# Kernel optimization log

Hardware: AMD Instinct MI355X
Metric: run time of the kernel (lower is better)

Reference implementation:

```python
import jax, jax.numpy as jnp
import numpy as np

COST_CLASS, COST_BBOX, COST_GIOU = 1.0, 5.0, 2.0
NUM_FRAMES, Q_PER_FRAME, NUM_TGT, NUM_CLASSES = 36, 100, 20, 92
B = 64


def box_cxcywh_to_xyxy(b):
    cx, cy, w, h = b[..., 0], b[..., 1], b[..., 2], b[..., 3]
    return jnp.stack([cx - 0.5 * w, cy - 0.5 * h, cx + 0.5 * w, cy + 0.5 * h], axis=-1)


def pairwise_giou(b1, b2):
    # b1: [..., Q, 4], b2: [..., T, 4], xyxy -> giou [..., Q, T]
    area1 = (b1[..., 2] - b1[..., 0]) * (b1[..., 3] - b1[..., 1])
    area2 = (b2[..., 2] - b2[..., 0]) * (b2[..., 3] - b2[..., 1])
    lt = jnp.maximum(b1[..., :, None, :2], b2[..., None, :, :2])
    rb = jnp.minimum(b1[..., :, None, 2:], b2[..., None, :, 2:])
    wh = jnp.clip(rb - lt, 0.0)
    inter = wh[..., 0] * wh[..., 1]
    union = area1[..., :, None] + area2[..., None, :] - inter
    iou = inter / union
    lt_e = jnp.minimum(b1[..., :, None, :2], b2[..., None, :, :2])
    rb_e = jnp.maximum(b1[..., :, None, 2:], b2[..., None, :, 2:])
    wh_e = jnp.clip(rb_e - lt_e, 0.0)
    area_e = wh_e[..., 0] * wh_e[..., 1]
    return iou - (area_e - union) / area_e


def compute_cost(pred_logits, pred_boxes, tgt_labels, tgt_boxes):
    b = pred_logits.shape[0]
    prob = jax.nn.softmax(pred_logits.reshape(b, NUM_FRAMES, Q_PER_FRAME, -1), axis=-1)  # [B,F,Q,C]
    pb = pred_boxes.reshape(b, NUM_FRAMES, Q_PER_FRAME, 4)
    lab = jnp.transpose(tgt_labels, (1, 0, 2))            # [B,F,T]
    tb = jnp.transpose(tgt_boxes, (1, 0, 2, 3))           # [B,F,T,4]
    onehot = jax.nn.one_hot(lab, prob.shape[-1], dtype=prob.dtype)  # [B,F,T,C]
    cost_class = -jnp.einsum('bfqc,bftc->bfqt', prob, onehot)
    cost_bbox = jnp.abs(pb[:, :, :, None, :] - tb[:, :, None, :, :]).sum(-1)  # L1 cdist
    giou = pairwise_giou(box_cxcywh_to_xyxy(pb), box_cxcywh_to_xyxy(tb))
    return COST_CLASS * cost_class + COST_BBOX * cost_bbox - COST_GIOU * giou


def auction_assign(cost):
    # cost [Q, T]; returns obj_of [T]: query index assigned to each target.
    # eps-optimal auction algorithm (replaces scipy linear_sum_assignment).
    Q, T = cost.shape
    benefit = -cost.T  # [T, Q]
    spread = jnp.max(benefit) - jnp.min(benefit) + 1e-6
    eps = spread / 1000.0
    neg_inf = jnp.asarray(-1e30, cost.dtype)

    def cond(s):
        _, _, obj_of, it = s
        return jnp.logical_and(jnp.any(obj_of < 0), it < 20000)

    def body(s):
        price, owner, obj_of, it = s
        unassigned = obj_of < 0                       # [T]
        vals = benefit - price[None, :]               # [T, Q]
        top2v, top2i = jax.lax.top_k(vals, 2)
        best_obj = top2i[:, 0]                        # [T]
        bid = price[best_obj] + (top2v[:, 0] - top2v[:, 1]) + eps
        bid = jnp.where(unassigned, bid, neg_inf)
        best_bid = jnp.full((Q,), neg_inf, cost.dtype).at[best_obj].max(bid)
        pids = jnp.arange(T, dtype=jnp.int32)
        win = unassigned & (bid >= best_bid[best_obj])
        winner = jnp.full((Q,), T, jnp.int32).at[best_obj].min(jnp.where(win, pids, T))
        has_bid = winner < T
        # evict previous owners of objects that received a bid
        evict = jnp.where(has_bid & (owner >= 0), owner, T)
        obj_of = obj_of.at[evict].set(-1, mode='drop')
        qids = jnp.arange(Q, dtype=jnp.int32)
        obj_of = obj_of.at[jnp.where(has_bid, winner, T)].set(jnp.where(has_bid, qids, -1), mode='drop')
        price = jnp.where(has_bid, best_bid, price)
        owner = jnp.where(has_bid, winner, owner)
        return price, owner, obj_of, it + 1

    init = (jnp.zeros((Q,), cost.dtype), jnp.full((Q,), -1, jnp.int32),
            jnp.full((T,), -1, jnp.int32), jnp.int32(0))
    _, _, obj_of, _ = jax.lax.while_loop(cond, body, init)
    return obj_of


def setup_inputs() -> dict:
    key = jax.random.key(0)
    k1, k2, k3, k4 = jax.random.split(key, 4)
    pred_logits = jax.random.normal(k1, (B, NUM_FRAMES * Q_PER_FRAME, NUM_CLASSES), jnp.float32)
    pred_boxes = jax.random.uniform(k2, (B, NUM_FRAMES * Q_PER_FRAME, 4), jnp.float32)
    tgt_labels = jax.random.randint(k3, (NUM_FRAMES, B, NUM_TGT), 0, NUM_CLASSES, jnp.int32)
    tgt_boxes = jax.random.uniform(k4, (NUM_FRAMES, B, NUM_TGT, 4), jnp.float32)
    return {'pred_logits': pred_logits, 'pred_boxes': pred_boxes,
            'tgt_labels': tgt_labels, 'tgt_boxes': tgt_boxes}


def reference(pred_logits, pred_boxes, tgt_labels, tgt_boxes):
    cost = compute_cost(pred_logits, pred_boxes, tgt_labels, tgt_boxes)  # [B,F,Q,T]
    b, f, q, t = cost.shape
    obj_of = jax.vmap(auction_assign)(cost.reshape(b * f, q, t))  # [BF, T]
    order = jnp.argsort(obj_of, axis=-1)  # scipy returns rows ascending
    pred_idx = jnp.take_along_axis(obj_of, order, axis=-1).reshape(b, f, t)
    tgt_idx = order.astype(jnp.int32).reshape(b, f, t)
    return cost, pred_idx, tgt_idx
```

## Files before the change

kernel.cpp:

```cpp
#include <hip/hip_runtime.h>

#define NF 36
#define QN 100
#define TN 20
#define CN 92
#define NB 64
#define BSTR 104

__global__ __launch_bounds__(64) void matcher_kernel(
    const float* __restrict__ logits,
    const float* __restrict__ pboxes,
    const int*   __restrict__ tlabels,
    const float* __restrict__ tboxes,
    float* __restrict__ out_cost,
    float* __restrict__ out_pred,
    float* __restrict__ out_tgt)
{
    const int bf = blockIdx.x;
    const int b  = bf / NF;
    const int f  = bf % NF;
    const int lane = threadIdx.x;

    __shared__ float ben[TN][BSTR];
    __shared__ float price[BSTR];
    __shared__ int   owner[QN];
    __shared__ float bidv[TN];
    __shared__ int   bo[TN];
    __shared__ int   evict[TN];
    __shared__ int   objl[TN];
    __shared__ int   slab[TN];
    __shared__ float tbr[TN][4];
    __shared__ float tbx[TN][4];
    __shared__ float tarea[TN];

    if (lane < TN) {
        const int base = (f * NB + b) * TN + lane;
        slab[lane] = tlabels[base];
        const float* tb = tboxes + (size_t)base * 4;
        float cx = tb[0], cy = tb[1], w = tb[2], h = tb[3];
        tbr[lane][0] = cx; tbr[lane][1] = cy; tbr[lane][2] = w; tbr[lane][3] = h;
        float x1 = cx - 0.5f * w, y1 = cy - 0.5f * h;
        float x2 = cx + 0.5f * w, y2 = cy + 0.5f * h;
        tbx[lane][0] = x1; tbx[lane][1] = y1; tbx[lane][2] = x2; tbx[lane][3] = y2;
        tarea[lane] = (x2 - x1) * (y2 - y1);
        evict[lane] = 0;
    }
    __syncthreads();

    float mn = INFINITY, mx = -INFINITY;
    for (int p = 0; p < 2; ++p) {
        const int q = lane + 64 * p;
        if (q < QN) {
            const size_t row = (size_t)b * (NF * QN) + (size_t)f * QN + q;
            const float* L = logits + row * CN;
            const float4* L4 = reinterpret_cast<const float4*>(L);
            float4 r[23];
            #pragma unroll
            for (int i = 0; i < 23; ++i) r[i] = L4[i];
            float m = -INFINITY;
            #pragma unroll
            for (int i = 0; i < 23; ++i) {
                float4 v = r[i];
                m = fmaxf(m, v.x); m = fmaxf(m, v.y); m = fmaxf(m, v.z); m = fmaxf(m, v.w);
            }
            float s = 0.f;
            #pragma unroll
            for (int i = 0; i < 23; ++i) {
                float4 v = r[i];
                s += expf(v.x - m); s += expf(v.y - m); s += expf(v.z - m); s += expf(v.w - m);
            }

            float4 pbv = reinterpret_cast<const float4*>(pboxes)[row];
            float cx = pbv.x, cy = pbv.y, w = pbv.z, h = pbv.w;
            float px1 = cx - 0.5f * w, py1 = cy - 0.5f * h;
            float px2 = cx + 0.5f * w, py2 = cy + 0.5f * h;
            float a1 = (px2 - px1) * (py2 - py1);

            for (int t = 0; t < TN; ++t) {
                float pc = expf(L[slab[t]] - m) / s;
                float cb = fabsf(cx - tbr[t][0]) + fabsf(cy - tbr[t][1]);
                cb = cb + fabsf(w - tbr[t][2]);
                cb = cb + fabsf(h - tbr[t][3]);
                float ltx = fmaxf(px1, tbx[t][0]), lty = fmaxf(py1, tbx[t][1]);
                float rbx = fminf(px2, tbx[t][2]), rby = fminf(py2, tbx[t][3]);
                float wx = fmaxf(rbx - ltx, 0.f), wy = fmaxf(rby - lty, 0.f);
                float inter = wx * wy;
                float uni = a1 + tarea[t] - inter;
                float iou = inter / uni;
                float ex1 = fminf(px1, tbx[t][0]), ey1 = fminf(py1, tbx[t][1]);
                float ex2 = fmaxf(px2, tbx[t][2]), ey2 = fmaxf(py2, tbx[t][3]);
                float ew = fmaxf(ex2 - ex1, 0.f), eh = fmaxf(ey2 - ey1, 0.f);
                float ae = ew * eh;
                float giou = iou - (ae - uni) / ae;
                float cost = (-pc) + 5.0f * cb - 2.0f * giou;
                ben[t][q] = -cost;
                mn = fminf(mn, cost);
                mx = fmaxf(mx, cost);
            }
        }
    }

    for (int i = lane; i < BSTR; i += 64) price[i] = 0.f;
    for (int i = lane; i < QN; i += 64) owner[i] = -1;
    if (lane < TN) {
        ben[lane][100] = -INFINITY; ben[lane][101] = -INFINITY;
        ben[lane][102] = -INFINITY; ben[lane][103] = -INFINITY;
    }
    __syncthreads();

    #pragma unroll
    for (int off = 32; off > 0; off >>= 1) {
        mn = fminf(mn, __shfl_xor(mn, off, 64));
        mx = fmaxf(mx, __shfl_xor(mx, off, 64));
    }
    const float eps = (((-mn) - (-mx)) + 1e-6f) / 1000.0f;

    {
        float4* dst = reinterpret_cast<float4*>(out_cost + (size_t)bf * (QN * TN));
        for (int i = lane; i < (QN * TN) / 4; i += 64) {
            int k = i * 4;
            int q = k / TN, t0 = k - q * TN;
            float4 v;
            v.x = -ben[t0 + 0][q]; v.y = -ben[t0 + 1][q];
            v.z = -ben[t0 + 2][q]; v.w = -ben[t0 + 3][q];
            dst[i] = v;
        }
    }

    const int myt = lane / 3;
    const int jj  = lane - myt * 3;
    const int q0  = jj * 34;
    const bool is_leader = (lane < 60) && (jj == 0);
    float breg[34];
    {
        const int tt = (lane < 60) ? myt : 0;
        #pragma unroll
        for (int k = 0; k < 34; ++k) breg[k] = ben[tt][q0 + k];
    }
    int myobj = -1;

    for (int it = 0; it < 20000; ++it) {
        unsigned long long U = __ballot(is_leader && (myobj < 0));
        if (U == 0ull) break;

        float v0 = -INFINITY, v1 = -INFINITY; int i0 = q0;
        #pragma unroll
        for (int k = 0; k < 34; ++k) {
            float v = breg[k] - price[q0 + k];
            bool c = v > v0;
            v1 = c ? v0 : fmaxf(v1, v);
            i0 = c ? (q0 + k) : i0;
            v0 = c ? v : v0;
        }
        {
            float av0 = __shfl_down(v0, 1), av1 = __shfl_down(v1, 1);
            int   ai0 = __shfl_down(i0, 1);
            float bv0 = __shfl_down(v0, 2), bv1 = __shfl_down(v1, 2);
            int   bi0 = __shfl_down(i0, 2);
            if (av0 > v0) { v1 = fmaxf(v0, av1); v0 = av0; i0 = ai0; }
            else          { v1 = fmaxf(av0, v1); }
            if (bv0 > v0) { v1 = fmaxf(v0, bv1); v0 = bv0; i0 = bi0; }
            else          { v1 = fmaxf(bv0, v1); }
        }
        float mybid = price[i0] + (v0 - v1) + eps;
        if (is_leader) { bidv[myt] = mybid; bo[myt] = i0; }
        __syncthreads();

        const bool act = is_leader && (((U >> lane) & 1ull) != 0ull);
        if (act) {
            bool lose = false;
            unsigned long long u = U;
            while (u) {
                int pos = __builtin_ctzll(u); u &= (u - 1);
                int t2 = pos / 3;
                if (t2 != myt) {
                    float bv = bidv[t2]; int ob = bo[t2];
                    lose = lose || (ob == i0 && (bv > mybid || (bv == mybid && t2 < myt)));
                }
            }
            if (!lose) {
                int q = i0;
                int old = owner[q];
                owner[q] = myt;
                price[q] = mybid;
                myobj = q;
                if (old >= 0) evict[old] = 1;
            }
        }
        __syncthreads();
        if (is_leader && evict[myt]) { myobj = -1; evict[myt] = 0; }
    }
    __syncthreads();
    if (is_leader) objl[myt] = myobj;
    __syncthreads();

    if (lane < TN) {
        int v = objl[lane];
        int r = 0;
        for (int u = 0; u < TN; ++u) {
            int w = objl[u];
            r += (w < v) || (w == v && u < lane);
        }
        out_pred[(size_t)bf * TN + r] = (float)v;
        out_tgt[(size_t)bf * TN + r]  = (float)lane;
    }
}

extern "C" void kernel_launch(void* const* d_in, const int* in_sizes, int n_in,
                              void* d_out, int out_size, void* d_ws, size_t ws_size,
                              hipStream_t stream) {
    const float* logits  = (const float*)d_in[0];
    const float* pboxes  = (const float*)d_in[1];
    const int*   tlabels = (const int*)d_in[2];
    const float* tboxes  = (const float*)d_in[3];

    float* out = (float*)d_out;
    float* out_cost = out;
    float* out_pred = out + (size_t)NB * NF * QN * TN;
    float* out_tgt  = out_pred + (size_t)NB * NF * TN;

    hipLaunchKernelGGL(matcher_kernel, dim3(NB * NF), dim3(64), 0, stream,
                       logits, pboxes, tlabels, tboxes, out_cost, out_pred, out_tgt);
}
```

Baseline: 180.3 us.

## Restructure auction loop with fast paths for few bidders and atomic conflict resolution

Adds a wave-wide top-2 search for the case of one or two unassigned targets, where all 64 lanes scan one target's row with float4 loads and xor shuffles. With a single bidder the conflict check is skipped entirely. With several bidders the serial scan over the ballot mask is replaced by shared-memory atomicMax/atomicMin on the float bits to pick the winner per object. Rows are padded to 112 and vectorised, with a med3-based top-2 update. This shortens the long tail of auction iterations where few targets remain, at the cost of extra barriers per iteration in the contested path.

```diff
diff --git a/kernel.cpp b/kernel.cpp
--- a/kernel.cpp
+++ b/kernel.cpp
@@ -5,7 +5,12 @@
 #define TN 20
 #define CN 92
 #define NB 64
-#define BSTR 104
+#define BSTR 112
+
+#define TOP2_STEP(VV, IDX) do { \
+    float v_ = (VV); bool c_ = v_ > v0; \
+    float nv1_ = __builtin_amdgcn_fmed3f(v_, v0, v1); \
+    i0 = c_ ? (IDX) : i0; v0 = fmaxf(v0, v_); v1 = nv1_; } while (0)
 
 __global__ __launch_bounds__(64) void matcher_kernel(
     const float* __restrict__ logits,
@@ -21,11 +26,11 @@
     const int f  = bf % NF;
     const int lane = threadIdx.x;
 
-    __shared__ float ben[TN][BSTR];
-    __shared__ float price[BSTR];
+    __shared__ __align__(16) float ben[TN][BSTR];
+    __shared__ __align__(16) float price[BSTR];
     __shared__ int   owner[QN];
-    __shared__ float bidv[TN];
-    __shared__ int   bo[TN];
+    __shared__ int   bbmax[QN];
+    __shared__ int   wmin[QN];
     __shared__ int   evict[TN];
     __shared__ int   objl[TN];
     __shared__ int   slab[TN];
@@ -103,8 +108,9 @@
     for (int i = lane; i < BSTR; i += 64) price[i] = 0.f;
     for (int i = lane; i < QN; i += 64) owner[i] = -1;
     if (lane < TN) {
-        ben[lane][100] = -INFINITY; ben[lane][101] = -INFINITY;
-        ben[lane][102] = -INFINITY; ben[lane][103] = -INFINITY;
+        float4 ninf; ninf.x = ninf.y = ninf.z = ninf.w = -INFINITY;
+        float4* sp = reinterpret_cast<float4*>(&ben[lane][100]);
+        sp[0] = ninf; sp[1] = ninf; sp[2] = ninf;
     }
     __syncthreads();
 
@@ -129,63 +135,102 @@
 
     const int myt = lane / 3;
     const int jj  = lane - myt * 3;
-    const int q0  = jj * 34;
+    const int q0  = jj * 36;
     const bool is_leader = (lane < 60) && (jj == 0);
-    float breg[34];
+    float4 breg4[9];
     {
         const int tt = (lane < 60) ? myt : 0;
+        const float4* bp = reinterpret_cast<const float4*>(&ben[tt][q0]);
         #pragma unroll
-        for (int k = 0; k < 34; ++k) breg[k] = ben[tt][q0 + k];
+        for (int k = 0; k < 9; ++k) breg4[k] = bp[k];
     }
     int myobj = -1;
 
     for (int it = 0; it < 20000; ++it) {
         unsigned long long U = __ballot(is_leader && (myobj < 0));
         if (U == 0ull) break;
-
-        float v0 = -INFINITY, v1 = -INFINITY; int i0 = q0;
-        #pragma unroll
-        for (int k = 0; k < 34; ++k) {
-            float v = breg[k] - price[q0 + k];
-            bool c = v > v0;
-            v1 = c ? v0 : fmaxf(v1, v);
-            i0 = c ? (q0 + k) : i0;
-            v0 = c ? v : v0;
-        }
-        {
-            float av0 = __shfl_down(v0, 1), av1 = __shfl_down(v1, 1);
-            int   ai0 = __shfl_down(i0, 1);
-            float bv0 = __shfl_down(v0, 2), bv1 = __shfl_down(v1, 2);
-            int   bi0 = __shfl_down(i0, 2);
-            if (av0 > v0) { v1 = fmaxf(v0, av1); v0 = av0; i0 = ai0; }
-            else          { v1 = fmaxf(av0, v1); }
-            if (bv0 > v0) { v1 = fmaxf(v0, bv1); v0 = bv0; i0 = bi0; }
-            else          { v1 = fmaxf(bv0, v1); }
-        }
-        float mybid = price[i0] + (v0 - v1) + eps;
-        if (is_leader) { bidv[myt] = mybid; bo[myt] = i0; }
-        __syncthreads();
-
-        const bool act = is_leader && (((U >> lane) & 1ull) != 0ull);
-        if (act) {
-            bool lose = false;
-            unsigned long long u = U;
-            while (u) {
-                int pos = __builtin_ctzll(u); u &= (u - 1);
-                int t2 = pos / 3;
-                if (t2 != myt) {
-                    float bv = bidv[t2]; int ob = bo[t2];
-                    lose = lose || (ob == i0 && (bv > mybid || (bv == mybid && t2 < myt)));
-                }
-            }
-            if (!lose) {
-                int q = i0;
-                int old = owner[q];
-                owner[q] = myt;
-                price[q] = mybid;
-                myobj = q;
-                if (old >= 0) evict[old] = 1;
-            }
+        const int u = __popcll(U);
+
+        int bidq = 0; float bidf = 0.f;
+        if (u > 2) {
+            float v0 = -INFINITY, v1 = -INFINITY; int i0 = q0;
+            const float4* pp = reinterpret_cast<const float4*>(&price[q0]);
+            #pragma unroll
+            for (int k = 0; k < 9; ++k) {
+                float4 bv = breg4[k];
+                float4 pv = pp[k];
+                TOP2_STEP(bv.x - pv.x, q0 + 4*k + 0);
+                TOP2_STEP(bv.y - pv.y, q0 + 4*k + 1);
+                TOP2_STEP(bv.z - pv.z, q0 + 4*k + 2);
+                TOP2_STEP(bv.w - pv.w, q0 + 4*k + 3);
+            }
+            {
+                float av0 = __shfl_down(v0, 1), av1 = __shfl_down(v1, 1);
+                int   ai0 = __shfl_down(i0, 1);
+                float bv0 = __shfl_down(v0, 2), bv1 = __shfl_down(v1, 2);
+                int   bi0 = __shfl_down(i0, 2);
+                if (av0 > v0) { v1 = fmaxf(v0, av1); v0 = av0; i0 = ai0; }
+                else          { v1 = fmaxf(av0, v1); }
+                if (bv0 > v0) { v1 = fmaxf(v0, bv1); v0 = bv0; i0 = bi0; }
+                else          { v1 = fmaxf(bv0, v1); }
+            }
+            bidq = i0;
+            bidf = price[i0] + (v0 - v1) + eps;
+        } else {
+            const int ta = (int)__builtin_ctzll(U) / 3;
+            const int tb = (u == 2) ? (int)__builtin_ctzll(U & (U - 1ull)) / 3 : ta;
+            const int grp = lane >> 5;
+            const int tg  = grp ? tb : ta;
+            const int l   = lane & 31;
+            const int lc  = (l > 25) ? 25 : l;
+            const int qb  = lc * 4;
+            float4 bv = *reinterpret_cast<const float4*>(&ben[tg][qb]);
+            float4 pv = *reinterpret_cast<const float4*>(&price[qb]);
+            float v0 = -INFINITY, v1 = -INFINITY; int i0 = qb;
+            TOP2_STEP(bv.x - pv.x, qb + 0);
+            TOP2_STEP(bv.y - pv.y, qb + 1);
+            TOP2_STEP(bv.z - pv.z, qb + 2);
+            TOP2_STEP(bv.w - pv.w, qb + 3);
+            #pragma unroll
+            for (int s = 16; s >= 1; s >>= 1) {
+                float av0 = __shfl_xor(v0, s), av1 = __shfl_xor(v1, s);
+                int   ai0 = __shfl_xor(i0, s);
+                bool take = (av0 > v0) || (av0 == v0 && ai0 < i0);
+                float nv1 = take ? fmaxf(v0, av1) : fmaxf(v1, av0);
+                v0 = take ? av0 : v0;
+                i0 = take ? ai0 : i0;
+                v1 = nv1;
+            }
+            float bidg = price[i0] + (v0 - v1) + eps;
+            float b0 = __shfl(bidg, 0),  b1 = __shfl(bidg, 32);
+            int   i0a = __shfl(i0, 0),   i0b = __shfl(i0, 32);
+            if (lane == 3 * ta)            { bidq = i0a; bidf = b0; }
+            if (u == 2 && lane == 3 * tb)  { bidq = i0b; bidf = b1; }
+        }
+
+        const bool act = is_leader && (myobj < 0);
+        bool win = false;
+        if (u == 1) {
+            win = act;
+        } else {
+            if (act) { bbmax[bidq] = 0; wmin[bidq] = 64; }
+            __syncthreads();
+            if (act) atomicMax(&bbmax[bidq], __float_as_int(bidf));
+            __syncthreads();
+            bool cand = false;
+            if (act) {
+                cand = (__float_as_int(bidf) >= bbmax[bidq]);
+                if (cand) atomicMin(&wmin[bidq], myt);
+            }
+            __syncthreads();
+            win = cand && (wmin[bidq] == myt);
+        }
+        if (win) {
+            int old = owner[bidq];
+            owner[bidq] = myt;
+            price[bidq] = bidf;
+            myobj = bidq;
+            if (old >= 0) evict[old] = 1;
         }
         __syncthreads();
         if (is_leader && evict[myt]) { myobj = -1; evict[myt] = 0; }
@@ -197,9 +242,9 @@
     if (lane < TN) {
         int v = objl[lane];
         int r = 0;
-        for (int u = 0; u < TN; ++u) {
-            int w = objl[u];
-            r += (w < v) || (w == v && u < lane);
+        for (int u2 = 0; u2 < TN; ++u2) {
+            int w = objl[u2];
+            r += (w < v) || (w == v && u2 < lane);
         }
         out_pred[(size_t)bf * TN + r] = (float)v;
         out_tgt[(size_t)bf * TN + r]  = (float)lane;
```

Measured after the change: 176.7 us. -2.0%, faster.

## Cache top-two auction candidates per target and drop block barriers in bidding

Applied to the files above, without the earlier changes.

The auction loop now caches each unassigned target's best and second-best query, with their benefits and prices. A full 108-entry rescan happens only when the cache is invalidated, either by a price change on the cached second-best query or by the best query losing its margin. Bids are packed into one 64-bit shared word. The owner and evict arrays, plus the __syncthreads calls, are removed, since eviction is now detected by scanning the packed bids of the same single-wavefront block. The layout is widened to 36 queries per lane with float4 loads, and a register-pinning asm is added around the softmax loads. Exchanges: more complex invalidation logic and a reliance on wavefront-synchronous LDS ordering, which could subtly change assignment results if the cache or ordering assumptions are wrong.

```diff
diff --git a/kernel.cpp b/kernel.cpp
--- a/kernel.cpp
+++ b/kernel.cpp
@@ -5,7 +5,31 @@
 #define TN 20
 #define CN 92
 #define NB 64
-#define BSTR 104
+#define BSTR 112
+
+#define SCAN6(BV, PV, IDX) do { \
+    float v_ = (BV) - (PV); \
+    bool c_ = v_ > v0; \
+    bool d_ = v_ > v1; \
+    float nv1_ = __builtin_amdgcn_fmed3f(v_, v0, v1); \
+    i1 = c_ ? i0 : (d_ ? (IDX) : i1); \
+    b1 = c_ ? b0 : (d_ ? (BV) : b1); \
+    v1 = nv1_; \
+    i0 = c_ ? (IDX) : i0; \
+    b0 = c_ ? (BV) : b0; \
+    v0 = fmaxf(v0, v_); } while (0)
+
+#define MERGE6(NV0, NI0, NB0, NV1, NI1, NB1) do { \
+    bool t_  = (NV0) > v0; \
+    bool s1_ = (NV1) > v0; \
+    bool s2_ = (NV0) > v1; \
+    float mv1_ = t_ ? (s1_ ? (NV1) : v0) : (s2_ ? (NV0) : v1); \
+    int   mi1_ = t_ ? (s1_ ? (NI1) : i0) : (s2_ ? (NI0) : i1); \
+    float mb1_ = t_ ? (s1_ ? (NB1) : b0) : (s2_ ? (NB0) : b1); \
+    v0 = t_ ? (NV0) : v0; \
+    i0 = t_ ? (NI0) : i0; \
+    b0 = t_ ? (NB0) : b0; \
+    v1 = mv1_; i1 = mi1_; b1 = mb1_; } while (0)
 
 __global__ __launch_bounds__(64) void matcher_kernel(
     const float* __restrict__ logits,
@@ -21,12 +45,9 @@
     const int f  = bf % NF;
     const int lane = threadIdx.x;
 
-    __shared__ float ben[TN][BSTR];
-    __shared__ float price[BSTR];
-    __shared__ int   owner[QN];
-    __shared__ float bidv[TN];
-    __shared__ int   bo[TN];
-    __shared__ int   evict[TN];
+    __shared__ __align__(16) float ben[TN][BSTR];
+    __shared__ __align__(16) float price[BSTR];
+    __shared__ unsigned long long bid2[TN];
     __shared__ int   objl[TN];
     __shared__ int   slab[TN];
     __shared__ float tbr[TN][4];
@@ -43,7 +64,6 @@
         float x2 = cx + 0.5f * w, y2 = cy + 0.5f * h;
         tbx[lane][0] = x1; tbx[lane][1] = y1; tbx[lane][2] = x2; tbx[lane][3] = y2;
         tarea[lane] = (x2 - x1) * (y2 - y1);
-        evict[lane] = 0;
     }
     __syncthreads();
 
@@ -57,6 +77,10 @@
             float4 r[23];
             #pragma unroll
             for (int i = 0; i < 23; ++i) r[i] = L4[i];
+            #pragma unroll
+            for (int i = 0; i < 23; ++i) {
+                asm volatile("" : "+v"(r[i].x), "+v"(r[i].y), "+v"(r[i].z), "+v"(r[i].w));
+            }
             float m = -INFINITY;
             #pragma unroll
             for (int i = 0; i < 23; ++i) {
@@ -101,10 +125,10 @@
     }
 
     for (int i = lane; i < BSTR; i += 64) price[i] = 0.f;
-    for (int i = lane; i < QN; i += 64) owner[i] = -1;
     if (lane < TN) {
-        ben[lane][100] = -INFINITY; ben[lane][101] = -INFINITY;
-        ben[lane][102] = -INFINITY; ben[lane][103] = -INFINITY;
+        float4 ninf; ninf.x = ninf.y = ninf.z = ninf.w = -INFINITY;
+        float4* sp = reinterpret_cast<float4*>(&ben[lane][100]);
+        sp[0] = ninf; sp[1] = ninf; sp[2] = ninf;
     }
     __syncthreads();
 
@@ -129,66 +153,96 @@
 
     const int myt = lane / 3;
     const int jj  = lane - myt * 3;
-    const int q0  = jj * 34;
+    const int q0  = jj * 36;
     const bool is_leader = (lane < 60) && (jj == 0);
-    float breg[34];
+    float4 breg4[9];
     {
         const int tt = (lane < 60) ? myt : 0;
+        const float4* bp = reinterpret_cast<const float4*>(&ben[tt][q0]);
         #pragma unroll
-        for (int k = 0; k < 34; ++k) breg[k] = ben[tt][q0 + k];
+        for (int k = 0; k < 9; ++k) breg4[k] = bp[k];
     }
     int myobj = -1;
+
+    float cv0 = 0.f, cv1 = 0.f, cb0 = 0.f, cb1 = 0.f, cp0 = 0.f;
+    int ci0 = 0, ci1 = 0;
+    bool cval = false;
 
     for (int it = 0; it < 20000; ++it) {
         unsigned long long U = __ballot(is_leader && (myobj < 0));
         if (U == 0ull) break;
-
-        float v0 = -INFINITY, v1 = -INFINITY; int i0 = q0;
-        #pragma unroll
-        for (int k = 0; k < 34; ++k) {
-            float v = breg[k] - price[q0 + k];
-            bool c = v > v0;
-            v1 = c ? v0 : fmaxf(v1, v);
-            i0 = c ? (q0 + k) : i0;
-            v0 = c ? v : v0;
-        }
-        {
-            float av0 = __shfl_down(v0, 1), av1 = __shfl_down(v1, 1);
-            int   ai0 = __shfl_down(i0, 1);
-            float bv0 = __shfl_down(v0, 2), bv1 = __shfl_down(v1, 2);
-            int   bi0 = __shfl_down(i0, 2);
-            if (av0 > v0) { v1 = fmaxf(v0, av1); v0 = av0; i0 = ai0; }
-            else          { v1 = fmaxf(av0, v1); }
-            if (bv0 > v0) { v1 = fmaxf(v0, bv1); v0 = bv0; i0 = bi0; }
-            else          { v1 = fmaxf(bv0, v1); }
-        }
-        float mybid = price[i0] + (v0 - v1) + eps;
-        if (is_leader) { bidv[myt] = mybid; bo[myt] = i0; }
-        __syncthreads();
-
-        const bool act = is_leader && (((U >> lane) & 1ull) != 0ull);
-        if (act) {
-            bool lose = false;
-            unsigned long long u = U;
-            while (u) {
-                int pos = __builtin_ctzll(u); u &= (u - 1);
+        unsigned long long R = __ballot(is_leader && (myobj < 0) && !cval);
+
+        if (R != 0ull) {
+            const bool doscan = (lane < 60) && (((R >> (3 * myt)) & 1ull) != 0ull);
+            float v0 = -INFINITY, v1 = -INFINITY, b0 = 0.f, b1 = 0.f;
+            int i0 = q0, i1 = q0;
+            if (doscan) {
+                const float4* pp = reinterpret_cast<const float4*>(&price[q0]);
+                #pragma unroll
+                for (int k = 0; k < 9; ++k) {
+                    float4 bv = breg4[k];
+                    float4 pv = pp[k];
+                    SCAN6(bv.x, pv.x, q0 + 4*k + 0);
+                    SCAN6(bv.y, pv.y, q0 + 4*k + 1);
+                    SCAN6(bv.z, pv.z, q0 + 4*k + 2);
+                    SCAN6(bv.w, pv.w, q0 + 4*k + 3);
+                }
+            }
+            {
+                float av0 = __shfl_down(v0, 1), av1 = __shfl_down(v1, 1);
+                float ab0 = __shfl_down(b0, 1), ab1 = __shfl_down(b1, 1);
+                int   ai0 = __shfl_down(i0, 1), ai1 = __shfl_down(i1, 1);
+                float bv0 = __shfl_down(v0, 2), bv1 = __shfl_down(v1, 2);
+                float bb0 = __shfl_down(b0, 2), bb1 = __shfl_down(b1, 2);
+                int   bi0 = __shfl_down(i0, 2), bi1 = __shfl_down(i1, 2);
+                MERGE6(av0, ai0, ab0, av1, ai1, ab1);
+                MERGE6(bv0, bi0, bb0, bv1, bi1, bb1);
+            }
+            if (is_leader && (((R >> lane) & 1ull) != 0ull)) {
+                cv0 = v0; ci0 = i0; cb0 = b0;
+                cv1 = v1; ci1 = i1; cb1 = b1;
+                cp0 = price[ci0];
+                cval = true;
+            }
+        }
+
+        const bool active = is_leader && (myobj < 0);
+        const int   mybidq = ci0;
+        const float mybid  = cp0 + (cv0 - cv1) + eps;
+        if (active) {
+            bid2[myt] = ((unsigned long long)__float_as_uint(mybid) << 32) | (unsigned)mybidq;
+        }
+
+        if (is_leader) {
+            bool lose = false, hit0 = false, kill = false, ev = false;
+            float np0 = -INFINITY;
+            unsigned long long uu = U;
+            while (uu) {
+                int pos = (int)__builtin_ctzll(uu); uu &= uu - 1ull;
                 int t2 = pos / 3;
-                if (t2 != myt) {
-                    float bv = bidv[t2]; int ob = bo[t2];
-                    lose = lose || (ob == i0 && (bv > mybid || (bv == mybid && t2 < myt)));
-                }
-            }
-            if (!lose) {
-                int q = i0;
-                int old = owner[q];
-                owner[q] = myt;
-                price[q] = mybid;
-                myobj = q;
-                if (old >= 0) evict[old] = 1;
-            }
-        }
-        __syncthreads();
-        if (is_leader && evict[myt]) { myobj = -1; evict[myt] = 0; }
+                unsigned long long pk = bid2[t2];
+                int q2 = (int)(unsigned)(pk & 0xffffffffull);
+                float f2 = __uint_as_float((unsigned)(pk >> 32));
+                lose = lose || (active && q2 == mybidq &&
+                                (f2 > mybid || (f2 == mybid && t2 < myt)));
+                ev = ev || (q2 == myobj);
+                bool h0 = (q2 == ci0);
+                np0 = h0 ? fmaxf(np0, f2) : np0;
+                hit0 = hit0 || h0;
+                kill = kill || (q2 == ci1);
+            }
+            if (active && !lose) {
+                myobj = mybidq;
+                price[mybidq] = mybid;
+            } else if (ev) {
+                myobj = -1;
+            }
+            if (cval) {
+                if (hit0) { cp0 = np0; cv0 = cb0 - cp0; }
+                if (kill || (hit0 && !(cv0 > cv1))) cval = false;
+            }
+        }
     }
     __syncthreads();
     if (is_leader) objl[myt] = myobj;
@@ -197,9 +251,9 @@
     if (lane < TN) {
         int v = objl[lane];
         int r = 0;
-        for (int u = 0; u < TN; ++u) {
-            int w = objl[u];
-            r += (w < v) || (w == v && u < lane);
+        for (int u2 = 0; u2 < TN; ++u2) {
+            int w = objl[u2];
+            r += (w < v) || (w == v && u2 < lane);
         }
         out_pred[(size_t)bf * TN + r] = (float)v;
         out_tgt[(size_t)bf * TN + r]  = (float)lane;
```

Result: slower. 184.7 us (+2.5%).
